# Kernel tuning notes

Measured on AMD Instinct MI355X. Metric: run time of the kernel, lower is better.

Reference implementation:

```python
import jax, jax.numpy as jnp
import numpy as np
import math

D_MODEL = 1024
NUM_HEADS = 16
D_K = D_MODEL // NUM_HEADS
THETA = 10000.0
BATCH = 2
SEQ = 2048


def setup_inputs() -> dict:
    key = jax.random.key(0)
    k = jax.random.split(key, 6)
    scale = 1.0 / math.sqrt(D_MODEL)
    in_features = jax.random.normal(k[0], (BATCH, SEQ, D_MODEL), dtype=jnp.float32)
    token_positions = jnp.sort(
        jax.random.randint(k[1], (BATCH, SEQ), 0, SEQ), axis=-1
    ).astype(jnp.int32)
    q_proj_weight = jax.random.normal(k[2], (D_MODEL, D_MODEL), dtype=jnp.float32) * scale
    k_proj_weight = jax.random.normal(k[3], (D_MODEL, D_MODEL), dtype=jnp.float32) * scale
    v_proj_weight = jax.random.normal(k[4], (D_MODEL, D_MODEL), dtype=jnp.float32) * scale
    o_proj_weight = jax.random.normal(k[5], (D_MODEL, D_MODEL), dtype=jnp.float32) * scale
    return {
        "in_features": in_features,
        "token_positions": token_positions,
        "q_proj_weight": q_proj_weight,
        "k_proj_weight": k_proj_weight,
        "v_proj_weight": v_proj_weight,
        "o_proj_weight": o_proj_weight,
    }


def _apply_rope(x, positions):
    # x: [b, h, s, d_k]; positions: [b, s]
    freqs = 1.0 / (THETA ** (jnp.arange(0, D_K, 2, dtype=jnp.float32) / D_K))  # [d_k/2]
    angles = positions[:, None, :, None].astype(jnp.float32) * freqs  # [b,1,s,d_k/2]
    cos, sin = jnp.cos(angles), jnp.sin(angles)
    x1 = x[..., 0::2]
    x2 = x[..., 1::2]
    x1r = x1 * cos - x2 * sin
    x2r = x1 * sin + x2 * cos
    # interleave pairs back: stack on new last axis then flatten
    return jnp.stack([x1r, x2r], axis=-1).reshape(x.shape)


def reference(in_features, token_positions, q_proj_weight, k_proj_weight,
              v_proj_weight, o_proj_weight):
    b, s, _ = in_features.shape
    Q = jnp.einsum('bsi,di->bsd', in_features, q_proj_weight)
    K = jnp.einsum('bsi,di->bsd', in_features, k_proj_weight)
    V = jnp.einsum('bsi,di->bsd', in_features, v_proj_weight)
    # split heads: [b, h, s, d_k]
    def split(x):
        return x.reshape(b, s, NUM_HEADS, D_K).transpose(0, 2, 1, 3)
    Q, K, V = split(Q), split(K), split(V)
    Q = _apply_rope(Q, token_positions)
    K = _apply_rope(K, token_positions)
    scores = jnp.einsum('bhqd,bhkd->bhqk', Q, K) / math.sqrt(D_K)
    causal = jnp.tril(jnp.ones((s, s), dtype=bool))  # allowed positions
    scores = jnp.where(causal[None, None], scores, -jnp.inf)
    weights = jax.nn.softmax(scores, axis=-1)
    head_out = jnp.einsum('bhqk,bhkd->bhqd', weights, V)
    combined = head_out.transpose(0, 2, 1, 3).reshape(b, s, D_MODEL)
    return jnp.einsum('bsd,od->bso', combined, o_proj_weight)
```

## Files before the change

kernel.cpp:

```cpp
#include <hip/hip_runtime.h>
#include <hip/hip_bf16.h>
#include <stdint.h>

#define DMODEL 1024
#define NH 16
#define DKH 64
#define BB 2
#define SS 2048
#define MTOT (BB*SS)

#define BM 128
#define BK 32
#define TP 136

using f32x4  = __attribute__((ext_vector_type(4))) float;
using bf16x8 = __attribute__((ext_vector_type(8))) __bf16;

#define GLL(g, l) __builtin_amdgcn_global_load_lds( \
    (const __attribute__((address_space(1))) unsigned int*)(g), \
    (__attribute__((address_space(3))) unsigned int*)(l), 16, 0, 0)

__device__ __forceinline__ unsigned short f2bf(float f) {
  union { float f; uint32_t u; } v; v.f = f;
  uint32_t r = v.u + 0x7FFFu + ((v.u >> 16) & 1u);
  return (unsigned short)(r >> 16);
}

__global__ __launch_bounds__(256) void cvt_all(
    const float* __restrict__ X,
    const float* __restrict__ w0, const float* __restrict__ w1,
    const float* __restrict__ w2, const float* __restrict__ w3,
    unsigned short* __restrict__ Xb,
    unsigned short* __restrict__ Wb)
{
  const int bid = blockIdx.x;
  const float* src;
  unsigned short* dst;
  int i;
  if (bid < 2048) {
    src = X; dst = Xb; i = bid * 256 + threadIdx.x;
  } else {
    int t = bid - 2048;
    int z = t >> 9;
    src = (z == 0) ? w0 : (z == 1) ? w1 : (z == 2) ? w2 : w3;
    dst = Wb + (size_t)z * DMODEL * DMODEL;
    i = (t & 511) * 256 + threadIdx.x;
  }
  const float4* s4 = (const float4*)src;
  float4 a = s4[2*i], b = s4[2*i+1];
  uint4 o;
  o.x = (uint32_t)f2bf(a.x) | ((uint32_t)f2bf(a.y) << 16);
  o.y = (uint32_t)f2bf(a.z) | ((uint32_t)f2bf(a.w) << 16);
  o.z = (uint32_t)f2bf(b.x) | ((uint32_t)f2bf(b.y) << 16);
  o.w = (uint32_t)f2bf(b.z) | ((uint32_t)f2bf(b.w) << 16);
  *(uint4*)(dst + (size_t)i * 8) = o;
}

template<int NI>
__device__ __forceinline__ void gemm_pipe(
    const unsigned short* __restrict__ A,
    const unsigned short* __restrict__ Bw,
    int m0, int n0, int K,
    unsigned short* As, unsigned short* Bs,
    f32x4 (&acc)[4][NI])
{
  const int BNl = NI * 32;
  const int tid = threadIdx.x;
  const int lane = tid & 63;
  const int w = tid >> 6;
  const int wr = w >> 1, wc = w & 1;
  const int lrow = lane & 15;
  const int g = lane >> 4;

  const f32x4 fzero = {0.f, 0.f, 0.f, 0.f};
  #pragma unroll
  for (int i = 0; i < 4; ++i)
    #pragma unroll
    for (int j = 0; j < NI; ++j)
      acc[i][j] = fzero;

  const int nk = K / BK;

  auto STAGE = [&](int k0, int buf) {
    #pragma unroll
    for (int c = 0; c < 2; ++c) {
      int i = tid + c * 256;
      int row = i >> 2, cc = i & 3;
      int sc = cc ^ ((row >> 1) & 3);
      GLL(A + (size_t)(m0 + row) * K + k0 + sc * 8, As + buf * (BM * BK) + i * 8);
    }
    #pragma unroll
    for (int c = 0; c < NI / 2; ++c) {
      int i = tid + c * 256;
      int row = i >> 2, cc = i & 3;
      int sc = cc ^ ((row >> 1) & 3);
      GLL(Bw + (size_t)(n0 + row) * K + k0 + sc * 8, Bs + buf * (BNl * BK) + i * 8);
    }
  };

  STAGE(0, 0);
  __syncthreads();
  for (int t = 0; t < nk; ++t) {
    const int cur = t & 1;
    if (t + 1 < nk) STAGE((t + 1) * BK, cur ^ 1);

    const unsigned short* Ab = As + cur * (BM * BK);
    const unsigned short* Bb = Bs + cur * (BNl * BK);
    bf16x8 af[4], bfr[NI];
    #pragma unroll
    for (int mi = 0; mi < 4; ++mi) {
      int row = wr * 64 + mi * 16 + lrow;
      af[mi] = *(const bf16x8*)(Ab + row * BK + (g ^ ((row >> 1) & 3)) * 8);
    }
    #pragma unroll
    for (int ni = 0; ni < NI; ++ni) {
      int row = wc * (NI * 16) + ni * 16 + lrow;
      bfr[ni] = *(const bf16x8*)(Bb + row * BK + (g ^ ((row >> 1) & 3)) * 8);
    }
    #pragma unroll
    for (int mi = 0; mi < 4; ++mi)
      #pragma unroll
      for (int ni = 0; ni < NI; ++ni)
        acc[mi][ni] = __builtin_amdgcn_mfma_f32_16x16x32_bf16(af[mi], bfr[ni], acc[mi][ni], 0, 0, 0);

    __syncthreads();
  }
}

__global__ __launch_bounds__(256) void gemm_qkv(
    const unsigned short* __restrict__ Xb,
    const unsigned short* __restrict__ Wf,
    const int* __restrict__ tpos,
    unsigned short* __restrict__ Qh,
    unsigned short* __restrict__ Kh,
    unsigned short* __restrict__ Vt)
{
  __shared__ __align__(16) unsigned char smraw[BM * TP * 2];
  unsigned short* sm = (unsigned short*)smraw;
  unsigned short* As = sm;
  unsigned short* Bs = sm + 2 * BM * BK;

  const int m0 = blockIdx.x * BM;
  const int n0 = blockIdx.y * 128;
  const int z  = n0 >> 10;
  const int nloc = n0 & 1023;

  f32x4 acc[4][4];
  gemm_pipe<4>(Xb, Wf, m0, n0, DMODEL, As, Bs, acc);

  const int tid  = threadIdx.x;
  const int lane = tid & 63;
  const int w    = tid >> 6;
  const int wr   = w >> 1, wc = w & 1;
  const int cb   = lane & 15, rb = (lane >> 4) * 4;

  if (z < 2) {
    #pragma unroll
    for (int mi = 0; mi < 4; ++mi)
      #pragma unroll
      for (int ni = 0; ni < 4; ++ni)
        #pragma unroll
        for (int r = 0; r < 4; ++r)
          sm[(wr * 64 + mi * 16 + rb + r) * TP + wc * 64 + ni * 16 + cb] = f2bf(acc[mi][ni][r]);
  } else {
    #pragma unroll
    for (int mi = 0; mi < 4; ++mi)
      #pragma unroll
      for (int ni = 0; ni < 4; ++ni)
        #pragma unroll
        for (int r = 0; r < 4; ++r)
          sm[(wc * 64 + ni * 16 + cb) * TP + wr * 64 + mi * 16 + rb + r] = f2bf(acc[mi][ni][r]);
  }
  __syncthreads();

  const int b = m0 >> 11;
  const float l2t = 13.28771237954945f / 32.0f;
  const float qsc = (z == 0) ? 0.18033688011112042f : 1.0f;

  if (z < 2) {
    unsigned short* dst = (z == 0) ? Qh : Kh;
    #pragma unroll
    for (int p = 0; p < 8; ++p) {
      const int m_l = p * 16 + (tid >> 4);
      const int ck  = tid & 15;
      bf16x8 vals = *(const bf16x8*)(sm + m_l * TP + ck * 8);
      const int m = m0 + m_l, s = m & (SS - 1);
      const int pos = tpos[m];
      const int n = nloc + ck * 8, h = n >> 6, dh = n & 63;
      union { unsigned short u[8]; uint4 v; } ov;
      #pragma unroll
      for (int e = 0; e < 4; ++e) {
        float x1 = (float)vals[2 * e], x2 = (float)vals[2 * e + 1];
        int j = (dh >> 1) + e;
        float ang = (float)pos * exp2f(-(float)j * l2t);
        float sn, cs;
        __sincosf(ang, &sn, &cs);
        sn *= qsc; cs *= qsc;
        ov.u[2 * e]     = f2bf(x1 * cs - x2 * sn);
        ov.u[2 * e + 1] = f2bf(x1 * sn + x2 * cs);
      }
      *(uint4*)(dst + ((size_t)(b * NH + h) * SS + s) * DKH + dh) = ov.v;
    }
  } else {
    #pragma unroll
    for (int p = 0; p < 8; ++p) {
      const int n_l = p * 16 + (tid >> 4);
      const int ck  = tid & 15;
      bf16x8 vals = *(const bf16x8*)(sm + n_l * TP + ck * 8);
      const int n = nloc + n_l, h = n >> 6, dh = n & 63;
      const int m = m0 + ck * 8, s = m & (SS - 1);
      *(bf16x8*)(Vt + ((size_t)(b * NH + h) * DKH + dh) * SS + s) = vals;
    }
  }
}

__global__ __launch_bounds__(256) void attn(
    const unsigned short* __restrict__ Qh,
    const unsigned short* __restrict__ Kh,
    const unsigned short* __restrict__ Vt,
    unsigned short* __restrict__ comb)
{
  __shared__ unsigned short Ks[2][64 * 64];
  __shared__ unsigned short Vs[2][64 * 64];
  __shared__ unsigned short Ps[4][16 * 64];

  const int idx = blockIdx.x;
  const int x = idx & 7;
  const int o = idx >> 3;
  const int g = o & 31;
  const int s = o >> 5;
  const int bh = x * 4 + s;
  const int g2 = (g + 8) & 31;
  const int qt = (s == 0) ? g : (s == 1) ? 31 - g : (s == 2) ? g2 : 31 - g2;

  const int tid = threadIdx.x, lane = tid & 63, w = tid >> 6;
  const int lc = lane & 15, lh = lane >> 4;

  const unsigned short* kb = Kh + (size_t)bh * SS * DKH;
  const unsigned short* vb = Vt + (size_t)bh * DKH * SS;
  const int b = bh >> 4, h = bh & 15;
  const f32x4 fzero = {0.f, 0.f, 0.f, 0.f};

  auto STAGE = [&](int t, int buf) {
    const int kv0 = t * 64;
    #pragma unroll
    for (int c = 0; c < 2; ++c) {
      int i = tid + c * 256;
      int row = i >> 3, pc = i & 7;
      int sc = pc ^ (row & 7);
      GLL(kb + (size_t)(kv0 + row) * DKH + sc * 8, &Ks[buf][i * 8]);
      GLL(vb + (size_t)row * SS + kv0 + sc * 8, &Vs[buf][i * 8]);
    }
  };

  const unsigned short* Qb = Qh + ((size_t)bh * SS + qt * 64 + w * 16 + lc) * DKH;
  bf16x8 qf0 = *(const bf16x8*)(Qb + lh * 8);
  bf16x8 qf1 = *(const bf16x8*)(Qb + lh * 8 + 32);

  f32x4 oacc[4];
  #pragma unroll
  for (int i = 0; i < 4; ++i) oacc[i] = fzero;
  float lsum = 0.f;
  unsigned short* psw = &Ps[w][0];

  auto QK = [&](int cur, f32x4 (&sacc)[4]) {
    __builtin_amdgcn_s_setprio(1);
    #pragma unroll
    for (int nf = 0; nf < 4; ++nf) {
      const int row = nf * 16 + lc;
      bf16x8 kf0 = *(const bf16x8*)(&Ks[cur][row * 64 + ((lh) ^ (row & 7)) * 8]);
      bf16x8 kf1 = *(const bf16x8*)(&Ks[cur][row * 64 + ((lh + 4) ^ (row & 7)) * 8]);
      sacc[nf] = __builtin_amdgcn_mfma_f32_16x16x32_bf16(kf0, qf0, fzero, 0, 0, 0);
      sacc[nf] = __builtin_amdgcn_mfma_f32_16x16x32_bf16(kf1, qf1, sacc[nf], 0, 0, 0);
    }
    __builtin_amdgcn_s_setprio(0);
  };

  auto SM = [&](f32x4 (&sacc)[4], bool domask, int t) {
    float sv[4][4];
    if (domask) {
      const int kv0 = t * 64;
      const int qlane = qt * 64 + w * 16 + lc;
      #pragma unroll
      for (int nf = 0; nf < 4; ++nf)
        #pragma unroll
        for (int r = 0; r < 4; ++r) {
          float x2 = sacc[nf][r];
          if ((kv0 + nf * 16 + lh * 4 + r) > qlane) x2 = -1e30f;
          sv[nf][r] = x2;
        }
    } else {
      #pragma unroll
      for (int nf = 0; nf < 4; ++nf)
        #pragma unroll
        for (int r = 0; r < 4; ++r)
          sv[nf][r] = sacc[nf][r];
    }
    float rs = 0.f;
    #pragma unroll
    for (int nf = 0; nf < 4; ++nf)
      #pragma unroll
      for (int r = 0; r < 4; ++r) {
        float p = exp2f(sv[nf][r]);
        sv[nf][r] = p;
        rs += p;
      }
    lsum += rs;
    #pragma unroll
    for (int nf = 0; nf < 4; ++nf) {
      uint32_t u0, u1;
      asm("v_cvt_pk_bf16_f32 %0, %1, %2" : "=v"(u0) : "v"(sv[nf][0]), "v"(sv[nf][1]));
      asm("v_cvt_pk_bf16_f32 %0, %1, %2" : "=v"(u1) : "v"(sv[nf][2]), "v"(sv[nf][3]));
      int swz = (nf * 2 + (lh >> 1)) ^ (lc & 7);
      uint32_t* p = (uint32_t*)&psw[lc * 64 + swz * 8 + (lh & 1) * 4];
      p[0] = u0; p[1] = u1;
    }
  };

  auto PV = [&](int cur) {
    __builtin_amdgcn_s_setprio(1);
    #pragma unroll
    for (int c = 0; c < 2; ++c) {
      bf16x8 pf = *(const bf16x8*)(&psw[lc * 64 + ((c * 4 + lh) ^ (lc & 7)) * 8]);
      #pragma unroll
      for (int df = 0; df < 4; ++df) {
        const int row = df * 16 + lc;
        bf16x8 vf = *(const bf16x8*)(&Vs[cur][row * 64 + ((c * 4 + lh) ^ (row & 7)) * 8]);
        oacc[df] = __builtin_amdgcn_mfma_f32_16x16x32_bf16(pf, vf, oacc[df], 0, 0, 0);
      }
    }
    __builtin_amdgcn_s_setprio(0);
  };

  STAGE(0, 0);
  for (int t = 0; t < qt; ++t) {
    const int cur = t & 1;
    asm volatile("s_waitcnt vmcnt(0)" ::: "memory");
    __builtin_amdgcn_s_barrier();
    f32x4 sacc[4];
    QK(cur, sacc);
    STAGE(t + 1, cur ^ 1);
    SM(sacc, false, t);
    PV(cur);
  }
  {
    const int cur = qt & 1;
    asm volatile("s_waitcnt vmcnt(0)" ::: "memory");
    __builtin_amdgcn_s_barrier();
    f32x4 sacc[4];
    QK(cur, sacc);
    SM(sacc, true, qt);
    PV(cur);
  }

  lsum += __shfl_xor(lsum, 16);
  lsum += __shfl_xor(lsum, 32);
  const int q0 = qt * 64;
  #pragma unroll
  for (int r = 0; r < 4; ++r) {
    float ls = __shfl(lsum, lh * 4 + r);
    float inv = 1.f / ls;
    const int q = q0 + w * 16 + lh * 4 + r;
    #pragma unroll
    for (int df = 0; df < 4; ++df) {
      const int d = h * 64 + df * 16 + lc;
      comb[((size_t)(b * SS + q)) * DMODEL + d] = f2bf(oacc[df][r] * inv);
    }
  }
}

__global__ __launch_bounds__(256) void gemm_out(
    const unsigned short* __restrict__ Cb,
    const unsigned short* __restrict__ Wob,
    float* __restrict__ out)
{
  __shared__ __align__(16) unsigned char smraw[BM * TP * 2];
  unsigned short* As = (unsigned short*)smraw;
  unsigned short* Bs = (unsigned short*)smraw + 2 * BM * BK;
  float* smf = (float*)smraw;

  const int m0 = blockIdx.x * BM, n0 = blockIdx.y * 64;
  f32x4 acc[4][2];
  gemm_pipe<2>(Cb, Wob, m0, n0, DMODEL, As, Bs, acc);

  const int tid  = threadIdx.x;
  const int lane = tid & 63;
  const int w    = tid >> 6;
  const int wr   = w >> 1, wc = w & 1;
  const int cb   = lane & 15, rb = (lane >> 4) * 4;

  #pragma unroll
  for (int mi = 0; mi < 4; ++mi)
    #pragma unroll
    for (int ni = 0; ni < 2; ++ni)
      #pragma unroll
      for (int r = 0; r < 4; ++r)
        smf[(wr * 64 + mi * 16 + rb + r) * 68 + wc * 32 + ni * 16 + cb] = acc[mi][ni][r];
  __syncthreads();

  #pragma unroll
  for (int p = 0; p < 8; ++p) {
    const int row = p * 16 + (tid >> 4);
    const int ck  = tid & 15;
    float4 vv = *(const float4*)(smf + row * 68 + ck * 4);
    *(float4*)(out + (size_t)(m0 + row) * DMODEL + n0 + ck * 4) = vv;
  }
}

extern "C" void kernel_launch(void* const* d_in, const int* in_sizes, int n_in,
                              void* d_out, int out_size, void* d_ws, size_t ws_size,
                              hipStream_t stream) {
  (void)in_sizes; (void)n_in; (void)out_size; (void)ws_size;
  const float* X    = (const float*)d_in[0];
  const int*   tpos = (const int*)d_in[1];
  const float* Wq   = (const float*)d_in[2];
  const float* Wk   = (const float*)d_in[3];
  const float* Wv   = (const float*)d_in[4];
  const float* Wo   = (const float*)d_in[5];
  float* out = (float*)d_out;

  uint8_t* ws = (uint8_t*)d_ws;
  const size_t SZ_X = (size_t)MTOT * DMODEL * 2;
  const size_t SZ_W = (size_t)DMODEL * DMODEL * 2;
  const size_t SZ_H = (size_t)BB * NH * SS * DKH * 2;
  unsigned short* Xb   = (unsigned short*)(ws);
  unsigned short* Wqb  = (unsigned short*)(ws + SZ_X);
  unsigned short* Wob  = (unsigned short*)(ws + SZ_X + 3 * SZ_W);
  unsigned short* Qh   = (unsigned short*)(ws + SZ_X + 4 * SZ_W);
  unsigned short* Kh   = (unsigned short*)(ws + SZ_X + 4 * SZ_W + SZ_H);
  unsigned short* Vt   = (unsigned short*)(ws + SZ_X + 4 * SZ_W + 2 * SZ_H);
  unsigned short* comb = Xb;

  cvt_all<<<dim3(4096), dim3(256), 0, stream>>>(X, Wq, Wk, Wv, Wo, Xb, Wqb);

  gemm_qkv<<<dim3(MTOT / BM, 24), dim3(256), 0, stream>>>(Xb, Wqb, tpos, Qh, Kh, Vt);
  attn<<<dim3(1024), dim3(256), 0, stream>>>(Qh, Kh, Vt, comb);
  gemm_out<<<dim3(MTOT / BM, 16), dim3(256), 0, stream>>>(comb, Wob, out);
}
```

Baseline: 111.3 us.

## Double attention query tile to 128 rows per block for K/V reuse

Each attention block now handles 128 query rows instead of 64: every wave computes two 16-row query groups that share each K/V tile loaded from LDS. The grid is halved to 512 blocks and the causal tile schedule is remapped so heavy and light query tiles are paired. The last two KV tiles are masked. The GEMM helper gains an MI template parameter, but both callers keep the same tile sizes. This halves K/V global and LDS traffic per query, at the cost of more registers, fewer blocks, and possible load imbalance.

```diff
diff --git a/kernel.cpp b/kernel.cpp
--- a/kernel.cpp
+++ b/kernel.cpp
@@ -9,7 +9,6 @@
 #define SS 2048
 #define MTOT (BB*SS)
 
-#define BM 128
 #define BK 32
 #define TP 136
 
@@ -56,14 +55,15 @@
   *(uint4*)(dst + (size_t)i * 8) = o;
 }
 
-template<int NI>
+template<int MI, int NI>
 __device__ __forceinline__ void gemm_pipe(
     const unsigned short* __restrict__ A,
     const unsigned short* __restrict__ Bw,
     int m0, int n0, int K,
     unsigned short* As, unsigned short* Bs,
-    f32x4 (&acc)[4][NI])
+    f32x4 (&acc)[MI][NI])
 {
+  const int BMl = MI * 32;
   const int BNl = NI * 32;
   const int tid = threadIdx.x;
   const int lane = tid & 63;
@@ -74,7 +74,7 @@
 
   const f32x4 fzero = {0.f, 0.f, 0.f, 0.f};
   #pragma unroll
-  for (int i = 0; i < 4; ++i)
+  for (int i = 0; i < MI; ++i)
     #pragma unroll
     for (int j = 0; j < NI; ++j)
       acc[i][j] = fzero;
@@ -83,11 +83,11 @@
 
   auto STAGE = [&](int k0, int buf) {
     #pragma unroll
-    for (int c = 0; c < 2; ++c) {
+    for (int c = 0; c < MI / 2; ++c) {
       int i = tid + c * 256;
       int row = i >> 2, cc = i & 3;
       int sc = cc ^ ((row >> 1) & 3);
-      GLL(A + (size_t)(m0 + row) * K + k0 + sc * 8, As + buf * (BM * BK) + i * 8);
+      GLL(A + (size_t)(m0 + row) * K + k0 + sc * 8, As + buf * (BMl * BK) + i * 8);
     }
     #pragma unroll
     for (int c = 0; c < NI / 2; ++c) {
@@ -104,12 +104,12 @@
     const int cur = t & 1;
     if (t + 1 < nk) STAGE((t + 1) * BK, cur ^ 1);
 
-    const unsigned short* Ab = As + cur * (BM * BK);
+    const unsigned short* Ab = As + cur * (BMl * BK);
     const unsigned short* Bb = Bs + cur * (BNl * BK);
-    bf16x8 af[4], bfr[NI];
-    #pragma unroll
-    for (int mi = 0; mi < 4; ++mi) {
-      int row = wr * 64 + mi * 16 + lrow;
+    bf16x8 af[MI], bfr[NI];
+    #pragma unroll
+    for (int mi = 0; mi < MI; ++mi) {
+      int row = wr * (MI * 16) + mi * 16 + lrow;
       af[mi] = *(const bf16x8*)(Ab + row * BK + (g ^ ((row >> 1) & 3)) * 8);
     }
     #pragma unroll
@@ -118,7 +118,7 @@
       bfr[ni] = *(const bf16x8*)(Bb + row * BK + (g ^ ((row >> 1) & 3)) * 8);
     }
     #pragma unroll
-    for (int mi = 0; mi < 4; ++mi)
+    for (int mi = 0; mi < MI; ++mi)
       #pragma unroll
       for (int ni = 0; ni < NI; ++ni)
         acc[mi][ni] = __builtin_amdgcn_mfma_f32_16x16x32_bf16(af[mi], bfr[ni], acc[mi][ni], 0, 0, 0);
@@ -135,18 +135,18 @@
     unsigned short* __restrict__ Kh,
     unsigned short* __restrict__ Vt)
 {
-  __shared__ __align__(16) unsigned char smraw[BM * TP * 2];
+  __shared__ __align__(16) unsigned char smraw[128 * TP * 2];
   unsigned short* sm = (unsigned short*)smraw;
   unsigned short* As = sm;
-  unsigned short* Bs = sm + 2 * BM * BK;
-
-  const int m0 = blockIdx.x * BM;
+  unsigned short* Bs = sm + 2 * 128 * BK;
+
+  const int m0 = blockIdx.x * 128;
   const int n0 = blockIdx.y * 128;
   const int z  = n0 >> 10;
   const int nloc = n0 & 1023;
 
   f32x4 acc[4][4];
-  gemm_pipe<4>(Xb, Wf, m0, n0, DMODEL, As, Bs, acc);
+  gemm_pipe<4, 4>(Xb, Wf, m0, n0, DMODEL, As, Bs, acc);
 
   const int tid  = threadIdx.x;
   const int lane = tid & 63;
@@ -222,16 +222,14 @@
 {
   __shared__ unsigned short Ks[2][64 * 64];
   __shared__ unsigned short Vs[2][64 * 64];
-  __shared__ unsigned short Ps[4][16 * 64];
+  __shared__ unsigned short Ps[4][32 * 64];
 
   const int idx = blockIdx.x;
   const int x = idx & 7;
   const int o = idx >> 3;
-  const int g = o & 31;
-  const int s = o >> 5;
-  const int bh = x * 4 + s;
-  const int g2 = (g + 8) & 31;
-  const int qt = (s == 0) ? g : (s == 1) ? 31 - g : (s == 2) ? g2 : 31 - g2;
+  const int bh = x * 4 + (o & 3);
+  const int j = o >> 2;
+  const int qt = (j < 8) ? j : 23 - j;
 
   const int tid = threadIdx.x, lane = tid & 63, w = tid >> 6;
   const int lc = lane & 15, lh = lane >> 4;
@@ -240,6 +238,7 @@
   const unsigned short* vb = Vt + (size_t)bh * DKH * SS;
   const int b = bh >> 4, h = bh & 15;
   const f32x4 fzero = {0.f, 0.f, 0.f, 0.f};
+  const int Q0 = qt * 128;
 
   auto STAGE = [&](int t, int buf) {
     const int kv0 = t * 64;
@@ -253,67 +252,79 @@
     }
   };
 
-  const unsigned short* Qb = Qh + ((size_t)bh * SS + qt * 64 + w * 16 + lc) * DKH;
-  bf16x8 qf0 = *(const bf16x8*)(Qb + lh * 8);
-  bf16x8 qf1 = *(const bf16x8*)(Qb + lh * 8 + 32);
-
-  f32x4 oacc[4];
-  #pragma unroll
-  for (int i = 0; i < 4; ++i) oacc[i] = fzero;
-  float lsum = 0.f;
+  bf16x8 qf[2][2];
+  #pragma unroll
+  for (int qg = 0; qg < 2; ++qg) {
+    const unsigned short* Qb = Qh + ((size_t)bh * SS + Q0 + w * 32 + qg * 16 + lc) * DKH;
+    qf[qg][0] = *(const bf16x8*)(Qb + lh * 8);
+    qf[qg][1] = *(const bf16x8*)(Qb + lh * 8 + 32);
+  }
+
+  f32x4 oacc[2][4];
+  #pragma unroll
+  for (int qg = 0; qg < 2; ++qg)
+    #pragma unroll
+    for (int i = 0; i < 4; ++i) oacc[qg][i] = fzero;
+  float lsum[2] = {0.f, 0.f};
   unsigned short* psw = &Ps[w][0];
 
-  auto QK = [&](int cur, f32x4 (&sacc)[4]) {
+  auto QK = [&](int cur, f32x4 (&sacc)[2][4]) {
     __builtin_amdgcn_s_setprio(1);
     #pragma unroll
     for (int nf = 0; nf < 4; ++nf) {
       const int row = nf * 16 + lc;
       bf16x8 kf0 = *(const bf16x8*)(&Ks[cur][row * 64 + ((lh) ^ (row & 7)) * 8]);
       bf16x8 kf1 = *(const bf16x8*)(&Ks[cur][row * 64 + ((lh + 4) ^ (row & 7)) * 8]);
-      sacc[nf] = __builtin_amdgcn_mfma_f32_16x16x32_bf16(kf0, qf0, fzero, 0, 0, 0);
-      sacc[nf] = __builtin_amdgcn_mfma_f32_16x16x32_bf16(kf1, qf1, sacc[nf], 0, 0, 0);
+      #pragma unroll
+      for (int qg = 0; qg < 2; ++qg) {
+        sacc[qg][nf] = __builtin_amdgcn_mfma_f32_16x16x32_bf16(kf0, qf[qg][0], fzero, 0, 0, 0);
+        sacc[qg][nf] = __builtin_amdgcn_mfma_f32_16x16x32_bf16(kf1, qf[qg][1], sacc[qg][nf], 0, 0, 0);
+      }
     }
     __builtin_amdgcn_s_setprio(0);
   };
 
-  auto SM = [&](f32x4 (&sacc)[4], bool domask, int t) {
-    float sv[4][4];
-    if (domask) {
-      const int kv0 = t * 64;
-      const int qlane = qt * 64 + w * 16 + lc;
+  auto SM = [&](f32x4 (&sacc)[2][4], bool domask, int t) {
+    #pragma unroll
+    for (int qg = 0; qg < 2; ++qg) {
+      float sv[4][4];
+      if (domask) {
+        const int kv0 = t * 64;
+        const int qlane = Q0 + w * 32 + qg * 16 + lc;
+        #pragma unroll
+        for (int nf = 0; nf < 4; ++nf)
+          #pragma unroll
+          for (int r = 0; r < 4; ++r) {
+            float x2 = sacc[qg][nf][r];
+            if ((kv0 + nf * 16 + lh * 4 + r) > qlane) x2 = -1e30f;
+            sv[nf][r] = x2;
+          }
+      } else {
+        #pragma unroll
+        for (int nf = 0; nf < 4; ++nf)
+          #pragma unroll
+          for (int r = 0; r < 4; ++r)
+            sv[nf][r] = sacc[qg][nf][r];
+      }
+      float rs = 0.f;
       #pragma unroll
       for (int nf = 0; nf < 4; ++nf)
         #pragma unroll
         for (int r = 0; r < 4; ++r) {
-          float x2 = sacc[nf][r];
-          if ((kv0 + nf * 16 + lh * 4 + r) > qlane) x2 = -1e30f;
-          sv[nf][r] = x2;
+          float p = exp2f(sv[nf][r]);
+          sv[nf][r] = p;
+          rs += p;
         }
-    } else {
-      #pragma unroll
-      for (int nf = 0; nf < 4; ++nf)
-        #pragma unroll
-        for (int r = 0; r < 4; ++r)
-          sv[nf][r] = sacc[nf][r];
-    }
-    float rs = 0.f;
-    #pragma unroll
-    for (int nf = 0; nf < 4; ++nf)
-      #pragma unroll
-      for (int r = 0; r < 4; ++r) {
-        float p = exp2f(sv[nf][r]);
-        sv[nf][r] = p;
-        rs += p;
-      }
-    lsum += rs;
-    #pragma unroll
-    for (int nf = 0; nf < 4; ++nf) {
-      uint32_t u0, u1;
-      asm("v_cvt_pk_bf16_f32 %0, %1, %2" : "=v"(u0) : "v"(sv[nf][0]), "v"(sv[nf][1]));
-      asm("v_cvt_pk_bf16_f32 %0, %1, %2" : "=v"(u1) : "v"(sv[nf][2]), "v"(sv[nf][3]));
-      int swz = (nf * 2 + (lh >> 1)) ^ (lc & 7);
-      uint32_t* p = (uint32_t*)&psw[lc * 64 + swz * 8 + (lh & 1) * 4];
-      p[0] = u0; p[1] = u1;
+      lsum[qg] += rs;
+      #pragma unroll
+      for (int nf = 0; nf < 4; ++nf) {
+        uint32_t u0, u1;
+        asm("v_cvt_pk_bf16_f32 %0, %1, %2" : "=v"(u0) : "v"(sv[nf][0]), "v"(sv[nf][1]));
+        asm("v_cvt_pk_bf16_f32 %0, %1, %2" : "=v"(u1) : "v"(sv[nf][2]), "v"(sv[nf][3]));
+        int swz = (nf * 2 + (lh >> 1)) ^ (lc & 7);
+        uint32_t* p = (uint32_t*)&psw[(qg * 16 + lc) * 64 + swz * 8 + (lh & 1) * 4];
+        p[0] = u0; p[1] = u1;
+      }
     }
   };
 
@@ -321,50 +332,62 @@
     __builtin_amdgcn_s_setprio(1);
     #pragma unroll
     for (int c = 0; c < 2; ++c) {
-      bf16x8 pf = *(const bf16x8*)(&psw[lc * 64 + ((c * 4 + lh) ^ (lc & 7)) * 8]);
+      bf16x8 pf[2];
+      #pragma unroll
+      for (int qg = 0; qg < 2; ++qg)
+        pf[qg] = *(const bf16x8*)(&psw[(qg * 16 + lc) * 64 + ((c * 4 + lh) ^ (lc & 7)) * 8]);
       #pragma unroll
       for (int df = 0; df < 4; ++df) {
         const int row = df * 16 + lc;
         bf16x8 vf = *(const bf16x8*)(&Vs[cur][row * 64 + ((c * 4 + lh) ^ (row & 7)) * 8]);
-        oacc[df] = __builtin_amdgcn_mfma_f32_16x16x32_bf16(pf, vf, oacc[df], 0, 0, 0);
+        #pragma unroll
+        for (int qg = 0; qg < 2; ++qg)
+          oacc[qg][df] = __builtin_amdgcn_mfma_f32_16x16x32_bf16(pf[qg], vf, oacc[qg][df], 0, 0, 0);
       }
     }
     __builtin_amdgcn_s_setprio(0);
   };
 
+  const int nt = 2 * qt + 2;
   STAGE(0, 0);
-  for (int t = 0; t < qt; ++t) {
+  for (int t = 0; t < 2 * qt; ++t) {
     const int cur = t & 1;
     asm volatile("s_waitcnt vmcnt(0)" ::: "memory");
     __builtin_amdgcn_s_barrier();
-    f32x4 sacc[4];
+    f32x4 sacc[2][4];
     QK(cur, sacc);
     STAGE(t + 1, cur ^ 1);
     SM(sacc, false, t);
     PV(cur);
   }
-  {
-    const int cur = qt & 1;
+  #pragma unroll
+  for (int tt = 0; tt < 2; ++tt) {
+    const int t = 2 * qt + tt;
+    const int cur = t & 1;
     asm volatile("s_waitcnt vmcnt(0)" ::: "memory");
     __builtin_amdgcn_s_barrier();
-    f32x4 sacc[4];
+    f32x4 sacc[2][4];
     QK(cur, sacc);
-    SM(sacc, true, qt);
+    if (t + 1 < nt) STAGE(t + 1, cur ^ 1);
+    SM(sacc, true, t);
     PV(cur);
   }
 
-  lsum += __shfl_xor(lsum, 16);
-  lsum += __shfl_xor(lsum, 32);
-  const int q0 = qt * 64;
-  #pragma unroll
-  for (int r = 0; r < 4; ++r) {
-    float ls = __shfl(lsum, lh * 4 + r);
-    float inv = 1.f / ls;
-    const int q = q0 + w * 16 + lh * 4 + r;
-    #pragma unroll
-    for (int df = 0; df < 4; ++df) {
-      const int d = h * 64 + df * 16 + lc;
-      comb[((size_t)(b * SS + q)) * DMODEL + d] = f2bf(oacc[df][r] * inv);
+  #pragma unroll
+  for (int qg = 0; qg < 2; ++qg) {
+    float ls0 = lsum[qg];
+    ls0 += __shfl_xor(ls0, 16);
+    ls0 += __shfl_xor(ls0, 32);
+    #pragma unroll
+    for (int r = 0; r < 4; ++r) {
+      float ls = __shfl(ls0, lh * 4 + r);
+      float inv = 1.f / ls;
+      const int q = Q0 + w * 32 + qg * 16 + lh * 4 + r;
+      #pragma unroll
+      for (int df = 0; df < 4; ++df) {
+        const int d = h * 64 + df * 16 + lc;
+        comb[((size_t)(b * SS + q)) * DMODEL + d] = f2bf(oacc[qg][df][r] * inv);
+      }
     }
   }
 }
@@ -374,14 +397,14 @@
     const unsigned short* __restrict__ Wob,
     float* __restrict__ out)
 {
-  __shared__ __align__(16) unsigned char smraw[BM * TP * 2];
+  __shared__ __align__(16) unsigned char smraw[128 * TP * 2];
   unsigned short* As = (unsigned short*)smraw;
-  unsigned short* Bs = (unsigned short*)smraw + 2 * BM * BK;
+  unsigned short* Bs = (unsigned short*)smraw + 2 * 128 * BK;
   float* smf = (float*)smraw;
 
-  const int m0 = blockIdx.x * BM, n0 = blockIdx.y * 64;
+  const int m0 = blockIdx.x * 128, n0 = blockIdx.y * 64;
   f32x4 acc[4][2];
-  gemm_pipe<2>(Cb, Wob, m0, n0, DMODEL, As, Bs, acc);
+  gemm_pipe<4, 2>(Cb, Wob, m0, n0, DMODEL, As, Bs, acc);
 
   const int tid  = threadIdx.x;
   const int lane = tid & 63;
@@ -433,7 +456,7 @@
 
   cvt_all<<<dim3(4096), dim3(256), 0, stream>>>(X, Wq, Wk, Wv, Wo, Xb, Wqb);
 
-  gemm_qkv<<<dim3(MTOT / BM, 24), dim3(256), 0, stream>>>(Xb, Wqb, tpos, Qh, Kh, Vt);
-  attn<<<dim3(1024), dim3(256), 0, stream>>>(Qh, Kh, Vt, comb);
-  gemm_out<<<dim3(MTOT / BM, 16), dim3(256), 0, stream>>>(comb, Wob, out);
-}
+  gemm_qkv<<<dim3(MTOT / 128, 24), dim3(256), 0, stream>>>(Xb, Wqb, tpos, Qh, Kh, Vt);
+  attn<<<dim3(512), dim3(256), 0, stream>>>(Qh, Kh, Vt, comb);
+  gemm_out<<<dim3(MTOT / 128, 16), dim3(256), 0, stream>>>(comb, Wob, out);
+}
```

Result: no change. 112.7 us (+1.3%).
